# Performance work log

Hardware: AMD Instinct MI355X
Metric: run time of the kernel (lower is better)

Reference implementation:

```python
import jax, jax.numpy as jnp
import numpy as np
import math

D_MODEL = 2048
D_STATE = 16
D_CONV = 4
EXPAND = 2
D_INNER = EXPAND * D_MODEL  # 4096, power of two for Hadamard
DT_RANK = math.ceil(D_MODEL / 16)  # 128
BATCH = 2
SEQLEN = 1024
DT_MIN, DT_MAX = 1e-3, 1e-1


def _hadamard_matrix(n):
    # Sylvester construction; n must be a power of two.
    H = np.array([[1.0]], dtype=np.float32)
    while H.shape[0] < n:
        H = np.block([[H, H], [H, -H]])
    return H

_H = jnp.asarray(_hadamard_matrix(D_INNER) / math.sqrt(D_INNER))


def setup_inputs() -> dict:
    key = jax.random.key(0)
    ks = jax.random.split(key, 10)
    hidden_states = jax.random.normal(ks[0], (BATCH, SEQLEN, D_MODEL), dtype=jnp.float32)
    # W4A16 linears behave as dense matmuls against dequantized weights.
    W_in = jax.random.normal(ks[1], (2 * D_INNER, D_MODEL), dtype=jnp.float32) * 0.02
    conv_w = jax.random.normal(ks[2], (D_INNER, D_CONV), dtype=jnp.float32) * 0.2
    conv_b = jax.random.normal(ks[3], (D_INNER,), dtype=jnp.float32) * 0.02
    W_x = jax.random.normal(ks[4], (DT_RANK + 2 * D_STATE, D_INNER), dtype=jnp.float32) * 0.02
    dt_init_std = DT_RANK ** -0.5
    W_dt = jax.random.uniform(ks[5], (D_INNER, DT_RANK), dtype=jnp.float32,
                              minval=-dt_init_std, maxval=dt_init_std)
    # dt_proj_bias init: inverse-softplus of dt sampled log-uniform in [dt_min, dt_max]
    u = jax.random.uniform(ks[6], (D_INNER,), dtype=jnp.float32)
    dt = jnp.clip(jnp.exp(u * (math.log(DT_MAX) - math.log(DT_MIN)) + math.log(DT_MIN)), 1e-4)
    dt_bias = dt + jnp.log(-jnp.expm1(-dt))
    A_log = jnp.log(jnp.broadcast_to(jnp.arange(1, D_STATE + 1, dtype=jnp.float32),
                                     (D_INNER, D_STATE)))
    D = jnp.ones((D_INNER,), dtype=jnp.float32)
    W_out = jax.random.normal(ks[7], (D_MODEL, D_INNER), dtype=jnp.float32) * 0.02
    return {"hidden_states": hidden_states, "W_in": W_in, "conv_w": conv_w,
            "conv_b": conv_b, "W_x": W_x, "W_dt": W_dt, "dt_bias": dt_bias,
            "A_log": A_log, "D": D, "W_out": W_out}


def _selective_scan(u, delta, A, Bm, Cm, D, z):
    # u, delta, z: (b, d, l); A: (d, n); Bm, Cm: (b, n, l); D: (d,)
    xs = (jnp.moveaxis(delta, 2, 0),          # (l, b, d)
          jnp.moveaxis(u, 2, 0),              # (l, b, d)
          jnp.moveaxis(Bm, 2, 0),             # (l, b, n)
          jnp.moveaxis(Cm, 2, 0))             # (l, b, n)
    b = u.shape[0]
    state0 = jnp.zeros((b, A.shape[0], A.shape[1]), dtype=u.dtype)

    def step(state, inp):
        dt_t, u_t, B_t, C_t = inp
        dA = jnp.exp(dt_t[:, :, None] * A[None])            # (b, d, n)
        dBu = (dt_t * u_t)[:, :, None] * B_t[:, None, :]     # (b, d, n)
        state = state * dA + dBu
        y_t = jnp.einsum('bdn,bn->bd', state, C_t)
        return state, y_t

    _, ys = jax.lax.scan(step, state0, xs)                   # ys: (l, b, d)
    y = jnp.moveaxis(ys, 0, 2)                               # (b, d, l)
    y = y + D[None, :, None] * u
    return y * jax.nn.silu(z)


def reference(hidden_states, W_in, conv_w, conv_b, W_x, W_dt, dt_bias, A_log, D, W_out):
    b, l, _ = hidden_states.shape
    # in_proj.to_seqlen_last -> (b, 2*d_inner, l)
    xz = jnp.einsum('bld,ed->bel', hidden_states, W_in)
    x, z = jnp.split(xz, 2, axis=1)                          # each (b, d_inner, l)
    # causal depthwise conv1d (left pad d_conv-1), then SiLU
    x = jax.lax.conv_general_dilated(
        x, conv_w[:, None, :], window_strides=(1,),
        padding=[(D_CONV - 1, 0)],
        dimension_numbers=('NCH', 'OIH', 'NCH'),
        feature_group_count=D_INNER)
    x = jax.nn.silu(x + conv_b[None, :, None])
    # x_proj -> dt, B, C
    x_dbl = jnp.einsum('bdl,ed->ble', x, W_x)                # (b, l, dt_rank+2n)
    dt_r, Bm, Cm = jnp.split(x_dbl, [DT_RANK, DT_RANK + D_STATE], axis=-1)
    delta = jnp.einsum('blr,dr->bdl', dt_r, W_dt)            # (b, d_inner, l)
    delta = jax.nn.softplus(delta + dt_bias[None, :, None])
    A = -jnp.exp(A_log)
    y = _selective_scan(x, delta, A,
                        jnp.moveaxis(Bm, 1, 2), jnp.moveaxis(Cm, 1, 2), D, z)
    y = jnp.moveaxis(y, 1, 2)                                # (b, l, d_inner)
    y = y @ _H                                               # normalized Hadamard
    return y @ W_out.T                                       # (b, l, d_model)
```

## Files before the change

### kernel.cpp

```cpp
#include <hip/hip_runtime.h>

#define B_   2
#define L_   1024
#define T_   2048
#define DM   2048
#define DI   4096
#define E2   8192
#define NS   16
#define RK   128
#define EX   160
#define SEG  16
#define SLEN (L_/SEG)
#define SLAB (B_*NS*DI)
#define MB(x) ((size_t)(x) << 20)

typedef __bf16 bf16x8 __attribute__((ext_vector_type(8)));
typedef float  f32x4  __attribute__((ext_vector_type(4)));

__device__ __forceinline__ float sigmoidf_(float x) { return 1.f / (1.f + __expf(-x)); }

__device__ __forceinline__ unsigned short bf_rne(float f) {
    unsigned int u = __float_as_uint(f);
    unsigned int r = u + 0x7fffu + ((u >> 16) & 1u);
    return (unsigned short)(r >> 16);
}
__device__ __forceinline__ float bf_to_f(unsigned short h) {
    return __uint_as_float(((unsigned int)h) << 16);
}
__device__ __forceinline__ float exp2_fast(float x) {
    float r;
    asm("v_exp_f32 %0, %1" : "=v"(r) : "v"(x));
    return r;
}

__global__ __launch_bounds__(256)
void split_bf16(const float* __restrict__ x, unsigned short* __restrict__ h,
                unsigned short* __restrict__ l, int n4)
{
    const int i = blockIdx.x * 256 + threadIdx.x;
    if (i >= n4) return;
    const float4 v = ((const float4*)x)[i];
    ushort4 hv, lv;
    hv.x = bf_rne(v.x); lv.x = bf_rne(v.x - bf_to_f(hv.x));
    hv.y = bf_rne(v.y); lv.y = bf_rne(v.y - bf_to_f(hv.y));
    hv.z = bf_rne(v.z); lv.z = bf_rne(v.z - bf_to_f(hv.z));
    hv.w = bf_rne(v.w); lv.w = bf_rne(v.w - bf_to_f(hv.w));
    ((ushort4*)h)[i] = hv;
    ((ushort4*)l)[i] = lv;
}

__global__ __launch_bounds__(256)
void gemm_bf16x3(const unsigned short* __restrict__ Ah, const unsigned short* __restrict__ Al,
                 const unsigned short* __restrict__ Bh, const unsigned short* __restrict__ Bl,
                 float* __restrict__ C, int K, int lda, int ldb, int ldc)
{
    __shared__ unsigned short lsAh[4096], lsAl[4096], lsBh[4096], lsBl[4096];
    const int bm   = blockIdx.y * 128;
    const int bn   = blockIdx.x * 128;
    const int tid  = threadIdx.x;
    const int lane = tid & 63;
    const int wv   = tid >> 6;
    const int wr   = (wv >> 1) * 64;
    const int wc   = (wv & 1) * 64;
    const int grow = lane >> 2;
    const int gcol = (lane & 3) * 8;
    const int fr   = lane & 15;
    const int fk   = (lane >> 4) * 8;

    f32x4 acc[4][4] = {};

    for (int k0 = 0; k0 < K; k0 += 32) {
        __syncthreads();
        #pragma unroll
        for (int is = 0; is < 2; ++is) {
            const int c = is * 4 + wv;
            const size_t ao = (size_t)(bm + c * 16 + grow) * lda + k0 + gcol;
            const size_t bo = (size_t)(bn + c * 16 + grow) * ldb + k0 + gcol;
            __builtin_amdgcn_global_load_lds((const __attribute__((address_space(1))) void*)(Ah + ao),
                (__attribute__((address_space(3))) void*)(lsAh + c * 512), 16, 0, 0);
            __builtin_amdgcn_global_load_lds((const __attribute__((address_space(1))) void*)(Al + ao),
                (__attribute__((address_space(3))) void*)(lsAl + c * 512), 16, 0, 0);
            __builtin_amdgcn_global_load_lds((const __attribute__((address_space(1))) void*)(Bh + bo),
                (__attribute__((address_space(3))) void*)(lsBh + c * 512), 16, 0, 0);
            __builtin_amdgcn_global_load_lds((const __attribute__((address_space(1))) void*)(Bl + bo),
                (__attribute__((address_space(3))) void*)(lsBl + c * 512), 16, 0, 0);
        }
        __syncthreads();

        bf16x8 ah[4], al[4], bh[4], bl[4];
        #pragma unroll
        for (int m = 0; m < 4; ++m) {
            const int ra = (wr + m * 16 + fr) * 32 + fk;
            ah[m] = *(const bf16x8*)(lsAh + ra);
            al[m] = *(const bf16x8*)(lsAl + ra);
        }
        #pragma unroll
        for (int n = 0; n < 4; ++n) {
            const int rb = (wc + n * 16 + fr) * 32 + fk;
            bh[n] = *(const bf16x8*)(lsBh + rb);
            bl[n] = *(const bf16x8*)(lsBl + rb);
        }
        #pragma unroll
        for (int m = 0; m < 4; ++m)
            #pragma unroll
            for (int n = 0; n < 4; ++n) {
                acc[m][n] = __builtin_amdgcn_mfma_f32_16x16x32_bf16(ah[m], bh[n], acc[m][n], 0, 0, 0);
                acc[m][n] = __builtin_amdgcn_mfma_f32_16x16x32_bf16(ah[m], bl[n], acc[m][n], 0, 0, 0);
                acc[m][n] = __builtin_amdgcn_mfma_f32_16x16x32_bf16(al[m], bh[n], acc[m][n], 0, 0, 0);
            }
    }

    #pragma unroll
    for (int m = 0; m < 4; ++m)
        #pragma unroll
        for (int n = 0; n < 4; ++n) {
            float* cp = C + (size_t)(bm + wr + m * 16 + (lane >> 4) * 4) * ldc
                          + bn + wc + n * 16 + fr;
            #pragma unroll
            for (int r = 0; r < 4; ++r) cp[(size_t)r * ldc] = acc[m][n][r];
        }
}

__global__ __launch_bounds__(256)
void gemm_xproj(const float* __restrict__ A, const float* __restrict__ B,
                float* __restrict__ C)
{
    __shared__ float As[16][132];
    __shared__ float Bs[16][36];
    const int bn    = blockIdx.x * 32;
    const int bm    = blockIdx.y * 128;
    const int kbase = blockIdx.z * 512;
    const int tid = threadIdx.x;
    const int tr  = tid >> 4;
    const int tc  = tid & 15;
    const int ar  = tid >> 2;
    const int ak  = (tid & 3) * 4;
    float acc[8][2] = {};
    for (int kc = 0; kc < 512; kc += 16) {
        const int k0 = kbase + kc;
        float4 a0 = *(const float4*)(A + (size_t)(bm + ar) * DI + k0 + ak);
        float4 a1 = *(const float4*)(A + (size_t)(bm + ar + 64) * DI + k0 + ak);
        float4 b0 = {0,0,0,0};
        if (tid < 128) b0 = *(const float4*)(B + (size_t)(bn + (tid >> 2)) * DI + k0 + ak);
        __syncthreads();
        As[ak+0][ar] = a0.x; As[ak+1][ar] = a0.y; As[ak+2][ar] = a0.z; As[ak+3][ar] = a0.w;
        As[ak+0][ar+64] = a1.x; As[ak+1][ar+64] = a1.y; As[ak+2][ar+64] = a1.z; As[ak+3][ar+64] = a1.w;
        if (tid < 128) {
            const int br = tid >> 2;
            Bs[ak+0][br] = b0.x; Bs[ak+1][br] = b0.y; Bs[ak+2][br] = b0.z; Bs[ak+3][br] = b0.w;
        }
        __syncthreads();
        #pragma unroll
        for (int k = 0; k < 16; ++k) {
            float af[8];
            *(float4*)&af[0] = *(const float4*)&As[k][tr*8];
            *(float4*)&af[4] = *(const float4*)&As[k][tr*8+4];
            const float bf0 = Bs[k][tc*2], bf1 = Bs[k][tc*2+1];
            #pragma unroll
            for (int i = 0; i < 8; ++i) {
                acc[i][0] = fmaf(af[i], bf0, acc[i][0]);
                acc[i][1] = fmaf(af[i], bf1, acc[i][1]);
            }
        }
    }
    #pragma unroll
    for (int i = 0; i < 8; ++i) {
        atomicAdd(&C[(size_t)(bm + tr*8 + i) * EX + bn + tc*2 + 0], acc[i][0]);
        atomicAdd(&C[(size_t)(bm + tr*8 + i) * EX + bn + tc*2 + 1], acc[i][1]);
    }
}

__global__ __launch_bounds__(256)
void conv_silu(const float* __restrict__ xz, const float* __restrict__ cw,
               const float* __restrict__ cb, float* __restrict__ xc)
{
    const int g   = blockIdx.x * 256 + threadIdx.x;
    const int nd4 = DI / 4;
    const int t   = g / nd4;
    const int d   = (g % nd4) * 4;
    const int l   = t & (L_ - 1);
    float w[4][4];
    #pragma unroll
    for (int c2 = 0; c2 < 4; ++c2) {
        float4 w4 = *(const float4*)(cw + (size_t)(d + c2) * 4);
        w[c2][0] = w4.x; w[c2][1] = w4.y; w[c2][2] = w4.z; w[c2][3] = w4.w;
    }
    float4 acc = *(const float4*)(cb + d);
    #pragma unroll
    for (int j = 0; j < 4; ++j) {
        const int lj = l + j - 3;
        if (lj >= 0) {
            const float4 x4 = *(const float4*)(xz + (size_t)(t + j - 3) * E2 + d);
            acc.x = fmaf(x4.x, w[0][j], acc.x);
            acc.y = fmaf(x4.y, w[1][j], acc.y);
            acc.z = fmaf(x4.z, w[2][j], acc.z);
            acc.w = fmaf(x4.w, w[3][j], acc.w);
        }
    }
    acc.x *= sigmoidf_(acc.x); acc.y *= sigmoidf_(acc.y);
    acc.z *= sigmoidf_(acc.z); acc.w *= sigmoidf_(acc.w);
    *(float4*)(xc + (size_t)t * DI + d) = acc;
}

__global__ __launch_bounds__(256)
void scan_passA(const float* __restrict__ u_in,
                const float* __restrict__ xdbl,
                const float* __restrict__ draw,
                const float* __restrict__ dt_bias,
                const float* __restrict__ A_log,
                float* __restrict__ pA, float* __restrict__ aB)
{
    __shared__ float sBl[SLEN * NS];
    const int d  = blockIdx.x * 256 + threadIdx.x;
    const int g  = blockIdx.y;
    const int b  = blockIdx.z;
    const int t0 = b * L_ + g * SLEN;

    for (int i = threadIdx.x; i < SLEN * NS; i += 256)
        sBl[i] = xdbl[(size_t)(t0 + (i >> 4)) * EX + RK + (i & 15)];
    __syncthreads();

    const float bias = dt_bias[d];
    float a2[NS], P[NS], S[NS];
    #pragma unroll
    for (int n = 0; n < NS; ++n) {
        a2[n] = -__expf(A_log[(size_t)d * NS + n]) * 1.44269504f;
        P[n] = 1.f; S[n] = 0.f;
    }
    for (int t = 0; t < SLEN; ++t) {
        const float dtr = draw[(size_t)(t0 + t) * DI + d];
        const float uu  = u_in[(size_t)(t0 + t) * DI + d];
        const float xv  = dtr + bias;
        const float dt  = fmaxf(xv, 0.f) + __logf(1.f + __expf(-fabsf(xv)));
        const float dtu = dt * uu;
        #pragma unroll
        for (int n = 0; n < NS; ++n) {
            const float e = exp2_fast(dt * a2[n]);
            P[n] *= e;
            S[n] = fmaf(S[n], e, dtu * sBl[(t << 4) | n]);
        }
    }
    const size_t base = (size_t)g * SLAB + (size_t)b * NS * DI + d;
    #pragma unroll
    for (int n = 0; n < NS; ++n) {
        pA[base + (size_t)n * DI] = P[n];
        aB[base + (size_t)n * DI] = S[n];
    }
}

__global__ __launch_bounds__(256)
void scan_combine(const float* __restrict__ pA, float* __restrict__ aB)
{
    const int j = blockIdx.x * 256 + threadIdx.x;
    float cum = aB[j];
    #pragma unroll
    for (int g = 1; g < SEG; ++g) {
        const size_t idx = (size_t)g * SLAB + j;
        cum = fmaf(pA[idx], cum, aB[idx]);
        aB[idx] = cum;
    }
}

__global__ __launch_bounds__(256)
void scan_passB(const float* __restrict__ u_in,
                const float* __restrict__ xdbl,
                const float* __restrict__ draw,
                const float* __restrict__ xz,
                const float* __restrict__ dt_bias,
                const float* __restrict__ A_log,
                const float* __restrict__ Dvec,
                const float* __restrict__ aB,
                float* __restrict__ y)
{
    __shared__ float sBl[SLEN * NS];
    __shared__ float sCl[SLEN * NS];
    const int d  = blockIdx.x * 256 + threadIdx.x;
    const int g  = blockIdx.y;
    const int b  = blockIdx.z;
    const int t0 = b * L_ + g * SLEN;

    for (int i = threadIdx.x; i < SLEN * NS; i += 256) {
        const size_t row = (size_t)(t0 + (i >> 4)) * EX + RK + (i & 15);
        sBl[i] = xdbl[row];
        sCl[i] = xdbl[row + NS];
    }
    __syncthreads();

    const float bias = dt_bias[d];
    const float Dd   = Dvec[d];
    float a2[NS], S[NS];
    #pragma unroll
    for (int n = 0; n < NS; ++n)
        a2[n] = -__expf(A_log[(size_t)d * NS + n]) * 1.44269504f;
    if (g == 0) {
        #pragma unroll
        for (int n = 0; n < NS; ++n) S[n] = 0.f;
    } else {
        const size_t base = (size_t)(g - 1) * SLAB + (size_t)b * NS * DI + d;
        #pragma unroll
        for (int n = 0; n < NS; ++n) S[n] = aB[base + (size_t)n * DI];
    }
    for (int t = 0; t < SLEN; ++t) {
        const float dtr = draw[(size_t)(t0 + t) * DI + d];
        const float uu  = u_in[(size_t)(t0 + t) * DI + d];
        const float zv  = xz  [(size_t)(t0 + t) * E2 + DI + d];
        const float xv  = dtr + bias;
        const float dt  = fmaxf(xv, 0.f) + __logf(1.f + __expf(-fabsf(xv)));
        const float dtu = dt * uu;
        float yv = 0.f;
        #pragma unroll
        for (int n = 0; n < NS; ++n) {
            const float e = exp2_fast(dt * a2[n]);
            S[n] = fmaf(S[n], e, dtu * sBl[(t << 4) | n]);
            yv   = fmaf(S[n], sCl[(t << 4) | n], yv);
        }
        yv = (yv + Dd * uu) * (zv * sigmoidf_(zv));
        y[(size_t)(t0 + t) * DI + d] = yv;
    }
}

__global__ __launch_bounds__(256)
void fwht_split(const float* __restrict__ y, unsigned short* __restrict__ h,
                unsigned short* __restrict__ l)
{
    __shared__ float ls[4096];
    const float* row = y + (size_t)blockIdx.x * DI;
    for (int i = threadIdx.x; i < 4096; i += 256) ls[i] = row[i];
    __syncthreads();
    for (int st = 0; st < 12; ++st) {
        const int stride = 1 << st;
        for (int k = threadIdx.x; k < 2048; k += 256) {
            const int i = ((k >> st) << (st + 1)) | (k & (stride - 1));
            const int j = i | stride;
            const float a = ls[i], b = ls[j];
            ls[i] = a + b; ls[j] = a - b;
        }
        __syncthreads();
    }
    const float sc = 1.0f / 64.0f;
    const size_t base = (size_t)blockIdx.x * DI;
    for (int i = threadIdx.x; i < 4096; i += 256) {
        const float v = ls[i] * sc;
        const unsigned short hb = bf_rne(v);
        h[base + i] = hb;
        l[base + i] = bf_rne(v - bf_to_f(hb));
    }
}

extern "C" void kernel_launch(void* const* d_in, const int* in_sizes, int n_in,
                              void* d_out, int out_size, void* d_ws, size_t ws_size,
                              hipStream_t stream)
{
    const float* hidden  = (const float*)d_in[0];
    const float* W_in    = (const float*)d_in[1];
    const float* conv_w  = (const float*)d_in[2];
    const float* conv_b  = (const float*)d_in[3];
    const float* W_x     = (const float*)d_in[4];
    const float* W_dt    = (const float*)d_in[5];
    const float* dt_bias = (const float*)d_in[6];
    const float* A_log   = (const float*)d_in[7];
    const float* Dvec    = (const float*)d_in[8];
    const float* W_out   = (const float*)d_in[9];
    float* out = (float*)d_out;

    char* ws = (char*)d_ws;
    float* xz   = (float*)(ws + MB(0));
    float* xc   = (float*)(ws + MB(64));
    float* xdbl = (float*)(ws + MB(96));
    float* draw = (float*)(ws + MB(98));
    float* ybuf = (float*)(ws + MB(130));
    unsigned short* hh  = (unsigned short*)(ws + MB(162));
    unsigned short* hl  = (unsigned short*)(ws + MB(170));
    unsigned short* wih = (unsigned short*)(ws + MB(98));
    unsigned short* wil = (unsigned short*)(ws + MB(130));
    unsigned short* xbh = (unsigned short*)(ws + MB(162));
    unsigned short* xbl = (unsigned short*)(ws + MB(163));
    unsigned short* wdh = (unsigned short*)(ws + MB(164));
    unsigned short* wdl = (unsigned short*)(ws + MB(165));
    float* pA = (float*)(ws + MB(166));
    float* aB = (float*)(ws + MB(176));
    unsigned short* woh = (unsigned short*)(ws + MB(166));
    unsigned short* wol = (unsigned short*)(ws + MB(182));
    unsigned short* yh  = (unsigned short*)(ws + MB(0));
    unsigned short* yl  = (unsigned short*)(ws + MB(16));

    const dim3 blk(256);

    split_bf16<<<dim3(4096),  blk, 0, stream>>>(hidden, hh, hl, T_ * DM / 4);
    split_bf16<<<dim3(16384), blk, 0, stream>>>(W_in, wih, wil, E2 * DM / 4);

    gemm_bf16x3<<<dim3(E2/128, T_/128), blk, 0, stream>>>(hh, hl, wih, wil, xz, DM, DM, DM, E2);

    conv_silu<<<dim3((T_ * (DI/4)) / 256), blk, 0, stream>>>(xz, conv_w, conv_b, xc);

    hipMemsetAsync(xdbl, 0, (size_t)T_ * EX * sizeof(float), stream);
    gemm_xproj<<<dim3(5, 16, 8), blk, 0, stream>>>(xc, W_x, xdbl);

    split_bf16<<<dim3(320), blk, 0, stream>>>(xdbl, xbh, xbl, T_ * EX / 4);
    split_bf16<<<dim3(512), blk, 0, stream>>>(W_dt, wdh, wdl, DI * RK / 4);
    gemm_bf16x3<<<dim3(DI/128, T_/128), blk, 0, stream>>>(xbh, xbl, wdh, wdl, draw, RK, EX, RK, DI);

    scan_passA<<<dim3(DI/256, SEG, B_), blk, 0, stream>>>(xc, xdbl, draw, dt_bias, A_log, pA, aB);
    scan_combine<<<dim3(SLAB/256), blk, 0, stream>>>(pA, aB);
    scan_passB<<<dim3(DI/256, SEG, B_), blk, 0, stream>>>(xc, xdbl, draw, xz, dt_bias, A_log,
                                                          Dvec, aB, ybuf);

    split_bf16<<<dim3(8192), blk, 0, stream>>>(W_out, woh, wol, DM * DI / 4);
    fwht_split<<<dim3(T_), blk, 0, stream>>>(ybuf, yh, yl);

    gemm_bf16x3<<<dim3(DM/128, T_/128), blk, 0, stream>>>(yh, yl, woh, wol, out, DI, DI, DI, DM);
}
```

Before: 759.5 us.

## Swizzle GEMM LDS layout and run x_proj on the bf16x3 MFMA GEMM

The shared-memory tiles of the bf16x3 MFMA GEMM now use an XOR swizzle on both the global-to-LDS load column and the fragment read offset, to remove LDS bank conflicts in the large in_proj and out_proj GEMMs. The fp32 SIMT split-K x_proj kernel, which used atomics and needed a memset, is replaced by the bf16x3 MFMA GEMM with a column bound on the output stores. conv_silu now also writes the hi/lo bf16 split of its output, so no separate split pass is needed. The new x_proj launch has only 32 blocks over K=4096, so it may underuse the GPU. Its B tile also reads past the 160 rows of W_x into unrelated workspace, though those results are masked out.

```diff
diff --git a/kernel.cpp b/kernel.cpp
--- a/kernel.cpp
+++ b/kernel.cpp
@@ -52,7 +52,7 @@
 __global__ __launch_bounds__(256)
 void gemm_bf16x3(const unsigned short* __restrict__ Ah, const unsigned short* __restrict__ Al,
                  const unsigned short* __restrict__ Bh, const unsigned short* __restrict__ Bl,
-                 float* __restrict__ C, int K, int lda, int ldb, int ldc)
+                 float* __restrict__ C, int K, int lda, int ldb, int ldc, int nmax)
 {
     __shared__ unsigned short lsAh[4096], lsAl[4096], lsBh[4096], lsBl[4096];
     const int bm   = blockIdx.y * 128;
@@ -63,9 +63,9 @@
     const int wr   = (wv >> 1) * 64;
     const int wc   = (wv & 1) * 64;
     const int grow = lane >> 2;
-    const int gcol = (lane & 3) * 8;
+    const int gcol = (((lane & 3) ^ ((lane >> 3) & 3)) * 8);
     const int fr   = lane & 15;
-    const int fk   = (lane >> 4) * 8;
+    const int ss   = lane >> 4;
 
     f32x4 acc[4][4] = {};
 
@@ -90,15 +90,17 @@
         bf16x8 ah[4], al[4], bh[4], bl[4];
         #pragma unroll
         for (int m = 0; m < 4; ++m) {
-            const int ra = (wr + m * 16 + fr) * 32 + fk;
-            ah[m] = *(const bf16x8*)(lsAh + ra);
-            al[m] = *(const bf16x8*)(lsAl + ra);
+            const int ra = wr + m * 16 + fr;
+            const int off = ra * 32 + ((ss ^ ((ra >> 1) & 3)) << 3);
+            ah[m] = *(const bf16x8*)(lsAh + off);
+            al[m] = *(const bf16x8*)(lsAl + off);
         }
         #pragma unroll
         for (int n = 0; n < 4; ++n) {
-            const int rb = (wc + n * 16 + fr) * 32 + fk;
-            bh[n] = *(const bf16x8*)(lsBh + rb);
-            bl[n] = *(const bf16x8*)(lsBl + rb);
+            const int rb = wc + n * 16 + fr;
+            const int off = rb * 32 + ((ss ^ ((rb >> 1) & 3)) << 3);
+            bh[n] = *(const bf16x8*)(lsBh + off);
+            bl[n] = *(const bf16x8*)(lsBl + off);
         }
         #pragma unroll
         for (int m = 0; m < 4; ++m)
@@ -114,65 +116,19 @@
     for (int m = 0; m < 4; ++m)
         #pragma unroll
         for (int n = 0; n < 4; ++n) {
-            float* cp = C + (size_t)(bm + wr + m * 16 + (lane >> 4) * 4) * ldc
-                          + bn + wc + n * 16 + fr;
-            #pragma unroll
-            for (int r = 0; r < 4; ++r) cp[(size_t)r * ldc] = acc[m][n][r];
-        }
-}
-
-__global__ __launch_bounds__(256)
-void gemm_xproj(const float* __restrict__ A, const float* __restrict__ B,
-                float* __restrict__ C)
-{
-    __shared__ float As[16][132];
-    __shared__ float Bs[16][36];
-    const int bn    = blockIdx.x * 32;
-    const int bm    = blockIdx.y * 128;
-    const int kbase = blockIdx.z * 512;
-    const int tid = threadIdx.x;
-    const int tr  = tid >> 4;
-    const int tc  = tid & 15;
-    const int ar  = tid >> 2;
-    const int ak  = (tid & 3) * 4;
-    float acc[8][2] = {};
-    for (int kc = 0; kc < 512; kc += 16) {
-        const int k0 = kbase + kc;
-        float4 a0 = *(const float4*)(A + (size_t)(bm + ar) * DI + k0 + ak);
-        float4 a1 = *(const float4*)(A + (size_t)(bm + ar + 64) * DI + k0 + ak);
-        float4 b0 = {0,0,0,0};
-        if (tid < 128) b0 = *(const float4*)(B + (size_t)(bn + (tid >> 2)) * DI + k0 + ak);
-        __syncthreads();
-        As[ak+0][ar] = a0.x; As[ak+1][ar] = a0.y; As[ak+2][ar] = a0.z; As[ak+3][ar] = a0.w;
-        As[ak+0][ar+64] = a1.x; As[ak+1][ar+64] = a1.y; As[ak+2][ar+64] = a1.z; As[ak+3][ar+64] = a1.w;
-        if (tid < 128) {
-            const int br = tid >> 2;
-            Bs[ak+0][br] = b0.x; Bs[ak+1][br] = b0.y; Bs[ak+2][br] = b0.z; Bs[ak+3][br] = b0.w;
-        }
-        __syncthreads();
-        #pragma unroll
-        for (int k = 0; k < 16; ++k) {
-            float af[8];
-            *(float4*)&af[0] = *(const float4*)&As[k][tr*8];
-            *(float4*)&af[4] = *(const float4*)&As[k][tr*8+4];
-            const float bf0 = Bs[k][tc*2], bf1 = Bs[k][tc*2+1];
-            #pragma unroll
-            for (int i = 0; i < 8; ++i) {
-                acc[i][0] = fmaf(af[i], bf0, acc[i][0]);
-                acc[i][1] = fmaf(af[i], bf1, acc[i][1]);
+            const int col = bn + wc + n * 16 + fr;
+            if (col < nmax) {
+                float* cp = C + (size_t)(bm + wr + m * 16 + (lane >> 4) * 4) * ldc + col;
+                #pragma unroll
+                for (int r = 0; r < 4; ++r) cp[(size_t)r * ldc] = acc[m][n][r];
             }
         }
-    }
-    #pragma unroll
-    for (int i = 0; i < 8; ++i) {
-        atomicAdd(&C[(size_t)(bm + tr*8 + i) * EX + bn + tc*2 + 0], acc[i][0]);
-        atomicAdd(&C[(size_t)(bm + tr*8 + i) * EX + bn + tc*2 + 1], acc[i][1]);
-    }
 }
 
 __global__ __launch_bounds__(256)
 void conv_silu(const float* __restrict__ xz, const float* __restrict__ cw,
-               const float* __restrict__ cb, float* __restrict__ xc)
+               const float* __restrict__ cb, float* __restrict__ xc,
+               unsigned short* __restrict__ xch, unsigned short* __restrict__ xcl)
 {
     const int g   = blockIdx.x * 256 + threadIdx.x;
     const int nd4 = DI / 4;
@@ -199,7 +155,15 @@
     }
     acc.x *= sigmoidf_(acc.x); acc.y *= sigmoidf_(acc.y);
     acc.z *= sigmoidf_(acc.z); acc.w *= sigmoidf_(acc.w);
-    *(float4*)(xc + (size_t)t * DI + d) = acc;
+    const size_t o = (size_t)t * DI + d;
+    *(float4*)(xc + o) = acc;
+    ushort4 hv, lv;
+    hv.x = bf_rne(acc.x); lv.x = bf_rne(acc.x - bf_to_f(hv.x));
+    hv.y = bf_rne(acc.y); lv.y = bf_rne(acc.y - bf_to_f(hv.y));
+    hv.z = bf_rne(acc.z); lv.z = bf_rne(acc.z - bf_to_f(hv.z));
+    hv.w = bf_rne(acc.w); lv.w = bf_rne(acc.w - bf_to_f(hv.w));
+    *(ushort4*)(xch + o) = hv;
+    *(ushort4*)(xcl + o) = lv;
 }
 
 __global__ __launch_bounds__(256)
@@ -373,14 +337,18 @@
     unsigned short* hl  = (unsigned short*)(ws + MB(170));
     unsigned short* wih = (unsigned short*)(ws + MB(98));
     unsigned short* wil = (unsigned short*)(ws + MB(130));
-    unsigned short* xbh = (unsigned short*)(ws + MB(162));
-    unsigned short* xbl = (unsigned short*)(ws + MB(163));
-    unsigned short* wdh = (unsigned short*)(ws + MB(164));
-    unsigned short* wdl = (unsigned short*)(ws + MB(165));
-    float* pA = (float*)(ws + MB(166));
-    float* aB = (float*)(ws + MB(176));
-    unsigned short* woh = (unsigned short*)(ws + MB(166));
-    unsigned short* wol = (unsigned short*)(ws + MB(182));
+    unsigned short* xch = (unsigned short*)(ws + MB(162));
+    unsigned short* xcl = (unsigned short*)(ws + MB(178));
+    unsigned short* wxh = (unsigned short*)(ws + MB(130));
+    unsigned short* wxl = (unsigned short*)(ws + MB(132));
+    unsigned short* xbh = (unsigned short*)(ws + MB(194));
+    unsigned short* xbl = (unsigned short*)(ws + MB(195));
+    unsigned short* wdh = (unsigned short*)(ws + MB(196));
+    unsigned short* wdl = (unsigned short*)(ws + MB(197));
+    float* pA = (float*)(ws + MB(162));
+    float* aB = (float*)(ws + MB(178));
+    unsigned short* woh = (unsigned short*)(ws + MB(162));
+    unsigned short* wol = (unsigned short*)(ws + MB(178));
     unsigned short* yh  = (unsigned short*)(ws + MB(0));
     unsigned short* yl  = (unsigned short*)(ws + MB(16));
 
@@ -389,16 +357,19 @@
     split_bf16<<<dim3(4096),  blk, 0, stream>>>(hidden, hh, hl, T_ * DM / 4);
     split_bf16<<<dim3(16384), blk, 0, stream>>>(W_in, wih, wil, E2 * DM / 4);
 
-    gemm_bf16x3<<<dim3(E2/128, T_/128), blk, 0, stream>>>(hh, hl, wih, wil, xz, DM, DM, DM, E2);
-
-    conv_silu<<<dim3((T_ * (DI/4)) / 256), blk, 0, stream>>>(xz, conv_w, conv_b, xc);
-
-    hipMemsetAsync(xdbl, 0, (size_t)T_ * EX * sizeof(float), stream);
-    gemm_xproj<<<dim3(5, 16, 8), blk, 0, stream>>>(xc, W_x, xdbl);
+    gemm_bf16x3<<<dim3(E2/128, T_/128), blk, 0, stream>>>(hh, hl, wih, wil, xz,
+                                                          DM, DM, DM, E2, E2);
+
+    conv_silu<<<dim3((T_ * (DI/4)) / 256), blk, 0, stream>>>(xz, conv_w, conv_b, xc, xch, xcl);
+
+    split_bf16<<<dim3(640), blk, 0, stream>>>(W_x, wxh, wxl, EX * DI / 4);
+    gemm_bf16x3<<<dim3(2, T_/128), blk, 0, stream>>>(xch, xcl, wxh, wxl, xdbl,
+                                                     DI, DI, DI, EX, EX);
 
     split_bf16<<<dim3(320), blk, 0, stream>>>(xdbl, xbh, xbl, T_ * EX / 4);
     split_bf16<<<dim3(512), blk, 0, stream>>>(W_dt, wdh, wdl, DI * RK / 4);
-    gemm_bf16x3<<<dim3(DI/128, T_/128), blk, 0, stream>>>(xbh, xbl, wdh, wdl, draw, RK, EX, RK, DI);
+    gemm_bf16x3<<<dim3(DI/128, T_/128), blk, 0, stream>>>(xbh, xbl, wdh, wdl, draw,
+                                                          RK, EX, RK, DI, DI);
 
     scan_passA<<<dim3(DI/256, SEG, B_), blk, 0, stream>>>(xc, xdbl, draw, dt_bias, A_log, pA, aB);
     scan_combine<<<dim3(SLAB/256), blk, 0, stream>>>(pA, aB);
@@ -408,5 +379,6 @@
     split_bf16<<<dim3(8192), blk, 0, stream>>>(W_out, woh, wol, DM * DI / 4);
     fwht_split<<<dim3(T_), blk, 0, stream>>>(ybuf, yh, yl);
 
-    gemm_bf16x3<<<dim3(DM/128, T_/128), blk, 0, stream>>>(yh, yl, woh, wol, out, DI, DI, DI, DM);
-}
+    gemm_bf16x3<<<dim3(DM/128, T_/128), blk, 0, stream>>>(yh, yl, woh, wol, out,
+                                                          DI, DI, DI, DM, DM);
+}
```

Measured after the change: 843.8 us. 11.1% more time.
